# Optimization experiments

Hardware: AMD Instinct MI355X
Metric: run time of the kernel (lower is better)

## Reference

```python
import jax, jax.numpy as jnp
import numpy as np

B, T, IN_F, F = 128, 256, 256, 256
TAU_MEM = 0.02
THRESH = 0.5
RESET = 0.0
BETA = 4.0
LN_EPS = 1e-6

# Fast-sigmoid surrogate spike: forward = Heaviside, backward = 1/(1+beta|x|)^2
@jax.custom_vjp
def spike_surrogate(x):
    return (x > 0.0).astype(x.dtype)

def _sp_fwd(x):
    return spike_surrogate(x), x

def _sp_bwd(x, g):
    return (g / jnp.square(1.0 + BETA * jnp.abs(x)),)

spike_surrogate.defvjp(_sp_fwd, _sp_bwd)


def setup_inputs() -> dict:
    key = jax.random.key(0)
    k0, k1 = jax.random.split(key)
    spikes = jax.random.uniform(k0, (B, T, IN_F), dtype=jnp.float32)
    W = jax.random.normal(k1, (IN_F, F), dtype=jnp.float32) / np.sqrt(IN_F)
    b = jnp.zeros((F,), jnp.float32)
    ln_scale = jnp.ones((T, F), jnp.float32)   # distinct LayerNorm per timestep
    ln_bias = jnp.zeros((T, F), jnp.float32)
    return {"spikes": spikes, "W": W, "b": b, "ln_scale": ln_scale, "ln_bias": ln_bias}


def reference(spikes, W, b, ln_scale, ln_bias):
    # Dense is shared across timesteps -> one big contraction, same math.
    currents = jnp.einsum('bti,if->btf', spikes, W) + b  # [B,T,F]
    alpha = jnp.exp(jnp.asarray(-1.0 / TAU_MEM, spikes.dtype))

    def step(v_mem, xs):
        cur, gamma, beta_ln = xs  # [B,F], [F], [F]
        v_mem = alpha * v_mem + (1.0 - alpha) * cur
        s = spike_surrogate(v_mem - THRESH)
        v_mem = v_mem * (1.0 - s) + RESET * s
        mu = jnp.mean(s, axis=-1, keepdims=True)
        var = jnp.var(s, axis=-1, keepdims=True)
        y = (s - mu) * jax.lax.rsqrt(var + LN_EPS) * gamma + beta_ln
        return v_mem, y

    v0 = jnp.zeros((spikes.shape[0], W.shape[1]), spikes.dtype)
    xs = (jnp.swapaxes(currents, 0, 1), ln_scale, ln_bias)  # time-major
    _, ys = jax.lax.scan(step, v0, xs)  # ys: [T,B,F]
    return jnp.swapaxes(ys, 0, 1)  # [B,T,F]
```

## Files before the change

### kernel.cpp

```cpp
#include <hip/hip_runtime.h>
#include <math.h>

#define NROWS 32768
#define NK 256
#define NF 256
#define NT_SEQ 256
#define MTILE 64
#define TAU 5e-4f


typedef __attribute__((ext_vector_type(4))) float f32x4;
typedef __attribute__((ext_vector_type(8))) _Float16 f16x8;

__device__ __forceinline__ unsigned short f16_bits(float x) {
    return __builtin_bit_cast(unsigned short, (_Float16)x);
}

__global__ void split_w(const float* __restrict__ W, unsigned short* __restrict__ wt) {
    const int k = blockIdx.x;
    const int col = threadIdx.x;
    const float w16 = W[k * NF + col] * 16.0f;
    const _Float16 h1 = (_Float16)w16;
    const float r = (w16 - (float)h1) * 2048.0f;
    const _Float16 h2 = (_Float16)r;
    const int ks = k >> 5, chunk = (k >> 3) & 3, j = k & 7;
    const int base = ((ks * 4 + chunk) * 2048) + col * 8 + j;
    wt[base] = __builtin_bit_cast(unsigned short, h1);
    wt[base + 65536] = __builtin_bit_cast(unsigned short, h2);
}

__global__ __launch_bounds__(512, 4)
void lif_main(const float* __restrict__ spikes,
              const float* __restrict__ W,
              const float* __restrict__ bias,
              const float* __restrict__ ln_scale,
              const float* __restrict__ ln_bias,
              const unsigned short* __restrict__ wt,
              float* __restrict__ out)
{
    __shared__ __align__(16) short alds[2][MTILE][264];
    __shared__ unsigned int bits[MTILE][8];
    __shared__ float rinv_s[MTILE], mu_s[MTILE];
    __shared__ unsigned int elist[96];
    __shared__ int ecnt;

    const int tid = threadIdx.x;
    const int lane = tid & 63;
    const int wid = tid >> 6;
    const int row0 = blockIdx.x * MTILE;

    if (tid == 0) ecnt = 0;

    #pragma unroll
    for (int it = 0; it < 8; ++it) {
        const int idx = it * 2048 + tid * 4;
        const int r = idx >> 8, c = idx & 255;
        const float4 v = *reinterpret_cast<const float4*>(
            spikes + (size_t)(row0 + r) * NK + c);
        unsigned short h[4], l[4];
        const float fv[4] = {v.x, v.y, v.z, v.w};
        #pragma unroll
        for (int e = 0; e < 4; ++e) {
            h[e] = f16_bits(fv[e]);
            const float hf = (float)__builtin_bit_cast(_Float16, h[e]);
            l[e] = f16_bits((fv[e] - hf) * 2048.0f);
        }
        *(uint2*)&alds[0][r][c] = make_uint2((unsigned int)h[0] | ((unsigned int)h[1] << 16),
                                             (unsigned int)h[2] | ((unsigned int)h[3] << 16));
        *(uint2*)&alds[1][r][c] = make_uint2((unsigned int)l[0] | ((unsigned int)l[1] << 16),
                                             (unsigned int)l[2] | ((unsigned int)l[3] << 16));
    }
    __syncthreads();

    f32x4 acc0[4][2], acc1[4][2];
    {
        const f32x4 z = {0.f, 0.f, 0.f, 0.f};
        #pragma unroll
        for (int mt = 0; mt < 4; ++mt)
            #pragma unroll
            for (int nt = 0; nt < 2; ++nt) { acc0[mt][nt] = z; acc1[mt][nt] = z; }
    }
    const int a_off = (lane & 15) * 264 + (lane >> 4) * 8;
    const int b_off = (lane >> 4) * 2048 + (wid * 32 + (lane & 15)) * 8;
    const short* alds_flat = &alds[0][0][0];

    #pragma unroll 2
    for (int ks = 0; ks < 8; ++ks) {
        f16x8 bf[2][2];
        #pragma unroll
        for (int c = 0; c < 2; ++c)
            #pragma unroll
            for (int nt = 0; nt < 2; ++nt)
                bf[c][nt] = *reinterpret_cast<const f16x8*>(
                    wt + c * 65536 + ks * 8192 + b_off + nt * 128);
        f16x8 ah[4], al[4];
        #pragma unroll
        for (int mt = 0; mt < 4; ++mt) {
            ah[mt] = *reinterpret_cast<const f16x8*>(
                alds_flat + (mt * 16) * 264 + ks * 32 + a_off);
            al[mt] = *reinterpret_cast<const f16x8*>(
                alds_flat + 16896 + (mt * 16) * 264 + ks * 32 + a_off);
        }
        #pragma unroll
        for (int mt = 0; mt < 4; ++mt)
            #pragma unroll
            for (int nt = 0; nt < 2; ++nt) {
                acc0[mt][nt] = __builtin_amdgcn_mfma_f32_16x16x32_f16(ah[mt], bf[0][nt], acc0[mt][nt], 0, 0, 0);
                acc1[mt][nt] = __builtin_amdgcn_mfma_f32_16x16x32_f16(ah[mt], bf[1][nt], acc1[mt][nt], 0, 0, 0);
                acc1[mt][nt] = __builtin_amdgcn_mfma_f32_16x16x32_f16(al[mt], bf[0][nt], acc1[mt][nt], 0, 0, 0);
            }
    }

    unsigned int smask[4] = {0u, 0u, 0u, 0u};
    #pragma unroll
    for (int mt = 0; mt < 4; ++mt)
        #pragma unroll
        for (int nt = 0; nt < 2; ++nt) {
            const int gcol = wid * 32 + nt * 16 + (lane & 15);
            const float bv = bias[gcol];
            #pragma unroll
            for (int reg = 0; reg < 4; ++reg) {
                const float v = fmaf(acc1[mt][nt][reg], 4.8828125e-4f,
                                     acc0[mt][nt][reg]) * 0.0625f + bv;
                if ((v - 0.5f) > 0.0f) smask[mt] |= 1u << (nt * 4 + reg);
                if (__builtin_expect(fabsf(v - 0.5f) < TAU, 0)) {
                    const int rl = mt * 16 + (lane >> 4) * 4 + reg;
                    const int ei = atomicAdd(&ecnt, 1);
                    if (ei < 96) elist[ei] = (unsigned int)((rl << 8) | gcol);
                }
            }
        }

    #pragma unroll
    for (int mt = 0; mt < 4; ++mt)
        #pragma unroll
        for (int reg = 0; reg < 4; ++reg) {
            const unsigned long long m0 = __ballot((smask[mt] >> (reg)) & 1u);
            const unsigned long long m1 = __ballot((smask[mt] >> (4 + reg)) & 1u);
            if (lane < 4) {
                const int g = lane;
                const unsigned int w =
                    (unsigned int)((m0 >> (g * 16)) & 0xFFFFull) |
                    ((unsigned int)((m1 >> (g * 16)) & 0xFFFFull) << 16);
                bits[mt * 16 + g * 4 + reg][wid] = w;
            }
        }
    __syncthreads();

    const int ne = min(ecnt, 96);
    for (int e = wid; e < ne; e += 8) {
        const unsigned int pk = elist[e];
        const int rl = (int)(pk >> 8), gcol = (int)(pk & 255u);
        const float* sr = spikes + (size_t)(row0 + rl) * NK;
        const float* wc = W + gcol;
        const int k0 = lane * 4;
        const double p0 = (double)sr[k0 + 0] * (double)wc[(size_t)(k0 + 0) * NF];
        const double p1 = (double)sr[k0 + 1] * (double)wc[(size_t)(k0 + 1) * NF];
        const double p2 = (double)sr[k0 + 2] * (double)wc[(size_t)(k0 + 2) * NF];
        const double p3 = (double)sr[k0 + 3] * (double)wc[(size_t)(k0 + 3) * NF];
        double pl = (p0 + p1) + (p2 + p3);
        #pragma unroll
        for (int off = 32; off > 0; off >>= 1) pl += __shfl_down(pl, off);
        if (lane == 0) {
            const double vex = pl + (double)bias[gcol];
            const bool sex = (vex - 0.5) > 0.0;
            const bool spv = (bits[rl][gcol >> 5] >> (gcol & 31)) & 1u;
            if (sex != spv) atomicXor(&bits[rl][gcol >> 5], 1u << (gcol & 31));
        }
    }
    __syncthreads();

    if (tid < MTILE) {
        int kc = 0;
        #pragma unroll
        for (int w = 0; w < 8; ++w) kc += __popc(bits[tid][w]);
        const double mu = (double)kc * (1.0 / 256.0);
        const double var = mu * (1.0 - mu);
        rinv_s[tid] = (float)(1.0 / sqrt(var + 1e-6));
        mu_s[tid] = (float)mu;
    }
    __syncthreads();

    const int orow = tid >> 3;
    const int of0 = (tid & 7) * 4;
    const int grow = row0 + orow;
    const int t = grow & (NT_SEQ - 1);
    const float rinv = rinv_s[orow];
    const float muf = mu_s[orow];
    #pragma unroll
    for (int j = 0; j < 8; ++j) {
        const int f = of0 + j * 32;
        const unsigned int wb = bits[orow][j];
        const int sh = of0;
        const float4 g4 = *reinterpret_cast<const float4*>(&ln_scale[t * NF + f]);
        const float4 b4 = *reinterpret_cast<const float4*>(&ln_bias[t * NF + f]);
        float4 o;
        const float s0 = ((wb >> (sh + 0)) & 1u) ? 1.0f : 0.0f;
        const float s1 = ((wb >> (sh + 1)) & 1u) ? 1.0f : 0.0f;
        const float s2 = ((wb >> (sh + 2)) & 1u) ? 1.0f : 0.0f;
        const float s3 = ((wb >> (sh + 3)) & 1u) ? 1.0f : 0.0f;
        o.x = (s0 - muf) * rinv * g4.x + b4.x;
        o.y = (s1 - muf) * rinv * g4.y + b4.y;
        o.z = (s2 - muf) * rinv * g4.z + b4.z;
        o.w = (s3 - muf) * rinv * g4.w + b4.w;
        *reinterpret_cast<float4*>(&out[(size_t)grow * NF + f]) = o;
    }
}

extern "C" void kernel_launch(void* const* d_in, const int* in_sizes, int n_in,
                              void* d_out, int out_size, void* d_ws, size_t ws_size,
                              hipStream_t stream) {
    const float* spikes   = (const float*)d_in[0];
    const float* W        = (const float*)d_in[1];
    const float* bias     = (const float*)d_in[2];
    const float* ln_scale = (const float*)d_in[3];
    const float* ln_bias  = (const float*)d_in[4];
    float* out = (float*)d_out;
    unsigned short* wt = (unsigned short*)d_ws;

    split_w<<<dim3(256), dim3(256), 0, stream>>>(W, wt);
    lif_main<<<dim3(NROWS / MTILE), dim3(512), 0, stream>>>(
        spikes, W, bias, ln_scale, ln_bias, wt, out);
}
```

Measured before the change: 36.52 us.

## Split LayerNorm epilogue into separate kernel using packed spike bits

Splits the fused kernel in two. The GEMM/threshold kernel now writes packed spike bitmasks and per-row mean/rsqrt stats to workspace. A new lightweight kernel then reads those, plus ln_scale and ln_bias, and writes the normalized output. The likely aim is to shorten the heavy kernel's tail and let the output stores run at their own occupancy, at the cost of an extra launch and a round trip through the workspace.

```diff
diff --git a/kernel.cpp b/kernel.cpp
--- a/kernel.cpp
+++ b/kernel.cpp
@@ -11,6 +11,10 @@
 
 typedef __attribute__((ext_vector_type(4))) float f32x4;
 typedef __attribute__((ext_vector_type(8))) _Float16 f16x8;
+
+#define WT_SHORTS  131072
+#define BITS_OFF   (WT_SHORTS * 2)
+#define STATS_OFF  (BITS_OFF + NROWS * 32)
 
 __device__ __forceinline__ unsigned short f16_bits(float x) {
     return __builtin_bit_cast(unsigned short, (_Float16)x);
@@ -30,17 +34,15 @@
 }
 
 __global__ __launch_bounds__(512, 4)
-void lif_main(const float* __restrict__ spikes,
+void lif_gemm(const float* __restrict__ spikes,
               const float* __restrict__ W,
               const float* __restrict__ bias,
-              const float* __restrict__ ln_scale,
-              const float* __restrict__ ln_bias,
               const unsigned short* __restrict__ wt,
-              float* __restrict__ out)
+              unsigned int* __restrict__ bitsg,
+              float2* __restrict__ stats)
 {
     __shared__ __align__(16) short alds[2][MTILE][264];
     __shared__ unsigned int bits[MTILE][8];
-    __shared__ float rinv_s[MTILE], mu_s[MTILE];
     __shared__ unsigned int elist[96];
     __shared__ int ecnt;
 
@@ -176,35 +178,40 @@
         for (int w = 0; w < 8; ++w) kc += __popc(bits[tid][w]);
         const double mu = (double)kc * (1.0 / 256.0);
         const double var = mu * (1.0 - mu);
-        rinv_s[tid] = (float)(1.0 / sqrt(var + 1e-6));
-        mu_s[tid] = (float)mu;
-    }
-    __syncthreads();
-
-    const int orow = tid >> 3;
-    const int of0 = (tid & 7) * 4;
-    const int grow = row0 + orow;
-    const int t = grow & (NT_SEQ - 1);
-    const float rinv = rinv_s[orow];
-    const float muf = mu_s[orow];
-    #pragma unroll
-    for (int j = 0; j < 8; ++j) {
-        const int f = of0 + j * 32;
-        const unsigned int wb = bits[orow][j];
-        const int sh = of0;
-        const float4 g4 = *reinterpret_cast<const float4*>(&ln_scale[t * NF + f]);
-        const float4 b4 = *reinterpret_cast<const float4*>(&ln_bias[t * NF + f]);
-        float4 o;
-        const float s0 = ((wb >> (sh + 0)) & 1u) ? 1.0f : 0.0f;
-        const float s1 = ((wb >> (sh + 1)) & 1u) ? 1.0f : 0.0f;
-        const float s2 = ((wb >> (sh + 2)) & 1u) ? 1.0f : 0.0f;
-        const float s3 = ((wb >> (sh + 3)) & 1u) ? 1.0f : 0.0f;
-        o.x = (s0 - muf) * rinv * g4.x + b4.x;
-        o.y = (s1 - muf) * rinv * g4.y + b4.y;
-        o.z = (s2 - muf) * rinv * g4.z + b4.z;
-        o.w = (s3 - muf) * rinv * g4.w + b4.w;
-        *reinterpret_cast<float4*>(&out[(size_t)grow * NF + f]) = o;
-    }
+        stats[row0 + tid] = make_float2((float)mu, (float)(1.0 / sqrt(var + 1e-6)));
+    }
+    const int rr = tid >> 3, w = tid & 7;
+    bitsg[(size_t)(row0 + rr) * 8 + w] = bits[rr][w];
+}
+
+__global__ __launch_bounds__(256)
+void lif_ln(const unsigned int* __restrict__ bitsg,
+            const float2* __restrict__ stats,
+            const float* __restrict__ ln_scale,
+            const float* __restrict__ ln_bias,
+            float* __restrict__ out)
+{
+    const int tid = threadIdx.x;
+    const int lane = tid & 63;
+    const int row = blockIdx.x * 4 + (tid >> 6);
+    const int t = row & (NT_SEQ - 1);
+    const float2 st = stats[row];
+    const unsigned int wb = bitsg[(size_t)row * 8 + (lane >> 3)];
+    const int f = lane * 4;
+    const int sh = f & 31;
+    const float4 g4 = *reinterpret_cast<const float4*>(&ln_scale[t * NF + f]);
+    const float4 b4 = *reinterpret_cast<const float4*>(&ln_bias[t * NF + f]);
+    const float muf = st.x, rinv = st.y;
+    float4 o;
+    const float s0 = ((wb >> (sh + 0)) & 1u) ? 1.0f : 0.0f;
+    const float s1 = ((wb >> (sh + 1)) & 1u) ? 1.0f : 0.0f;
+    const float s2 = ((wb >> (sh + 2)) & 1u) ? 1.0f : 0.0f;
+    const float s3 = ((wb >> (sh + 3)) & 1u) ? 1.0f : 0.0f;
+    o.x = (s0 - muf) * rinv * g4.x + b4.x;
+    o.y = (s1 - muf) * rinv * g4.y + b4.y;
+    o.z = (s2 - muf) * rinv * g4.z + b4.z;
+    o.w = (s3 - muf) * rinv * g4.w + b4.w;
+    *reinterpret_cast<float4*>(&out[(size_t)row * NF + f]) = o;
 }
 
 extern "C" void kernel_launch(void* const* d_in, const int* in_sizes, int n_in,
@@ -216,9 +223,14 @@
     const float* ln_scale = (const float*)d_in[3];
     const float* ln_bias  = (const float*)d_in[4];
     float* out = (float*)d_out;
+
     unsigned short* wt = (unsigned short*)d_ws;
+    unsigned int* bitsg = (unsigned int*)((char*)d_ws + BITS_OFF);
+    float2* stats = (float2*)((char*)d_ws + STATS_OFF);
 
     split_w<<<dim3(256), dim3(256), 0, stream>>>(W, wt);
-    lif_main<<<dim3(NROWS / MTILE), dim3(512), 0, stream>>>(
-        spikes, W, bias, ln_scale, ln_bias, wt, out);
-}
+    lif_gemm<<<dim3(NROWS / MTILE), dim3(512), 0, stream>>>(
+        spikes, W, bias, wt, bitsg, stats);
+    lif_ln<<<dim3(NROWS / 4), dim3(256), 0, stream>>>(
+        bitsg, stats, ln_scale, ln_bias, out);
+}
```

Result: slower. 40.75 us (+11.6%).

## Pipeline spike tile loading with MFMA compute across K chunks

Applied to the files above, without the earlier changes.

The up-front load and fp16 hi/lo split of the whole 64x256 spike tile is replaced by four 64-column chunks. Each next chunk's global loads are issued before the MFMAs on the current chunk, and the conversion and LDS writes happen after those MFMAs. The goal is to hide global-load latency behind matrix compute instead of stalling before the GEMM starts. In exchange it adds three extra block barriers, and because chunks are written in place while other waves may still be reading the same LDS buffer, correctness hinges on each chunk occupying a disjoint column range.

```diff
diff --git a/kernel.cpp b/kernel.cpp
--- a/kernel.cpp
+++ b/kernel.cpp
@@ -51,26 +51,36 @@
 
     if (tid == 0) ecnt = 0;
 
-    #pragma unroll
-    for (int it = 0; it < 8; ++it) {
-        const int idx = it * 2048 + tid * 4;
-        const int r = idx >> 8, c = idx & 255;
-        const float4 v = *reinterpret_cast<const float4*>(
-            spikes + (size_t)(row0 + r) * NK + c);
-        unsigned short h[4], l[4];
-        const float fv[4] = {v.x, v.y, v.z, v.w};
+    const int st_r0 = (tid) >> 4,          st_c0 = (tid & 15) * 4;
+    const int st_r1 = (512 + tid) >> 4,    st_c1 = (tid & 15) * 4;
+
+    const short* alds_flat = &alds[0][0][0];
+    short* alds_w = &alds[0][0][0];
+
+    auto cvt_write = [&](int chunk, const float4& va, const float4& vb) {
+        const float fv0[4] = {va.x, va.y, va.z, va.w};
+        const float fv1[4] = {vb.x, vb.y, vb.z, vb.w};
+        unsigned short h0[4], l0[4], h1[4], l1[4];
         #pragma unroll
         for (int e = 0; e < 4; ++e) {
-            h[e] = f16_bits(fv[e]);
-            const float hf = (float)__builtin_bit_cast(_Float16, h[e]);
-            l[e] = f16_bits((fv[e] - hf) * 2048.0f);
-        }
-        *(uint2*)&alds[0][r][c] = make_uint2((unsigned int)h[0] | ((unsigned int)h[1] << 16),
-                                             (unsigned int)h[2] | ((unsigned int)h[3] << 16));
-        *(uint2*)&alds[1][r][c] = make_uint2((unsigned int)l[0] | ((unsigned int)l[1] << 16),
-                                             (unsigned int)l[2] | ((unsigned int)l[3] << 16));
-    }
-    __syncthreads();
+            h0[e] = f16_bits(fv0[e]);
+            const float hf0 = (float)__builtin_bit_cast(_Float16, h0[e]);
+            l0[e] = f16_bits((fv0[e] - hf0) * 2048.0f);
+            h1[e] = f16_bits(fv1[e]);
+            const float hf1 = (float)__builtin_bit_cast(_Float16, h1[e]);
+            l1[e] = f16_bits((fv1[e] - hf1) * 2048.0f);
+        }
+        const int o0 = st_r0 * 264 + chunk * 64 + st_c0;
+        const int o1 = st_r1 * 264 + chunk * 64 + st_c1;
+        *(uint2*)&alds_w[o0] = make_uint2((unsigned int)h0[0] | ((unsigned int)h0[1] << 16),
+                                          (unsigned int)h0[2] | ((unsigned int)h0[3] << 16));
+        *(uint2*)&alds_w[16896 + o0] = make_uint2((unsigned int)l0[0] | ((unsigned int)l0[1] << 16),
+                                                  (unsigned int)l0[2] | ((unsigned int)l0[3] << 16));
+        *(uint2*)&alds_w[o1] = make_uint2((unsigned int)h1[0] | ((unsigned int)h1[1] << 16),
+                                          (unsigned int)h1[2] | ((unsigned int)h1[3] << 16));
+        *(uint2*)&alds_w[16896 + o1] = make_uint2((unsigned int)l1[0] | ((unsigned int)l1[1] << 16),
+                                                  (unsigned int)l1[2] | ((unsigned int)l1[3] << 16));
+    };
 
     f32x4 acc0[4][2], acc1[4][2];
     {
@@ -82,33 +92,58 @@
     }
     const int a_off = (lane & 15) * 264 + (lane >> 4) * 8;
     const int b_off = (lane >> 4) * 2048 + (wid * 32 + (lane & 15)) * 8;
-    const short* alds_flat = &alds[0][0][0];
-
-    #pragma unroll 2
-    for (int ks = 0; ks < 8; ++ks) {
-        f16x8 bf[2][2];
-        #pragma unroll
-        for (int c = 0; c < 2; ++c)
-            #pragma unroll
-            for (int nt = 0; nt < 2; ++nt)
-                bf[c][nt] = *reinterpret_cast<const f16x8*>(
-                    wt + c * 65536 + ks * 8192 + b_off + nt * 128);
-        f16x8 ah[4], al[4];
-        #pragma unroll
-        for (int mt = 0; mt < 4; ++mt) {
-            ah[mt] = *reinterpret_cast<const f16x8*>(
-                alds_flat + (mt * 16) * 264 + ks * 32 + a_off);
-            al[mt] = *reinterpret_cast<const f16x8*>(
-                alds_flat + 16896 + (mt * 16) * 264 + ks * 32 + a_off);
-        }
-        #pragma unroll
-        for (int mt = 0; mt < 4; ++mt)
-            #pragma unroll
-            for (int nt = 0; nt < 2; ++nt) {
-                acc0[mt][nt] = __builtin_amdgcn_mfma_f32_16x16x32_f16(ah[mt], bf[0][nt], acc0[mt][nt], 0, 0, 0);
-                acc1[mt][nt] = __builtin_amdgcn_mfma_f32_16x16x32_f16(ah[mt], bf[1][nt], acc1[mt][nt], 0, 0, 0);
-                acc1[mt][nt] = __builtin_amdgcn_mfma_f32_16x16x32_f16(al[mt], bf[0][nt], acc1[mt][nt], 0, 0, 0);
+
+    {
+        const float4 va = *reinterpret_cast<const float4*>(
+            spikes + (size_t)(row0 + st_r0) * NK + st_c0);
+        const float4 vb = *reinterpret_cast<const float4*>(
+            spikes + (size_t)(row0 + st_r1) * NK + st_c1);
+        cvt_write(0, va, vb);
+    }
+    __syncthreads();
+
+    #pragma unroll
+    for (int c = 0; c < 4; ++c) {
+        float4 va, vb;
+        if (c < 3) {
+            const int col_a = (c + 1) * 64 + st_c0;
+            const int col_b = (c + 1) * 64 + st_c1;
+            va = *reinterpret_cast<const float4*>(
+                spikes + (size_t)(row0 + st_r0) * NK + col_a);
+            vb = *reinterpret_cast<const float4*>(
+                spikes + (size_t)(row0 + st_r1) * NK + col_b);
+        }
+
+        #pragma unroll
+        for (int kk = 0; kk < 2; ++kk) {
+            const int ks = c * 2 + kk;
+            f16x8 bf[2][2];
+            #pragma unroll
+            for (int cc = 0; cc < 2; ++cc)
+                #pragma unroll
+                for (int nt = 0; nt < 2; ++nt)
+                    bf[cc][nt] = *reinterpret_cast<const f16x8*>(
+                        wt + cc * 65536 + ks * 8192 + b_off + nt * 128);
+            f16x8 ah[4], al[4];
+            #pragma unroll
+            for (int mt = 0; mt < 4; ++mt) {
+                ah[mt] = *reinterpret_cast<const f16x8*>(
+                    alds_flat + (mt * 16) * 264 + ks * 32 + a_off);
+                al[mt] = *reinterpret_cast<const f16x8*>(
+                    alds_flat + 16896 + (mt * 16) * 264 + ks * 32 + a_off);
             }
+            #pragma unroll
+            for (int mt = 0; mt < 4; ++mt)
+                #pragma unroll
+                for (int nt = 0; nt < 2; ++nt) {
+                    acc0[mt][nt] = __builtin_amdgcn_mfma_f32_16x16x32_f16(ah[mt], bf[0][nt], acc0[mt][nt], 0, 0, 0);
+                    acc1[mt][nt] = __builtin_amdgcn_mfma_f32_16x16x32_f16(ah[mt], bf[1][nt], acc1[mt][nt], 0, 0, 0);
+                    acc1[mt][nt] = __builtin_amdgcn_mfma_f32_16x16x32_f16(al[mt], bf[0][nt], acc1[mt][nt], 0, 0, 0);
+                }
+        }
+
+        if (c < 3) cvt_write(c + 1, va, vb);
+        __syncthreads();
     }
 
     unsigned int smask[4] = {0u, 0u, 0u, 0u};
```

Result: no change. 36.47 us (-0.1%).
